# Performance work log

Measured on AMD Instinct MI355X. Metric: run time of the kernel, lower is better.

## Reference

```python
import jax, jax.numpy as jnp
import numpy as np

K = 16  # buckets per block (2**treeDepth)
DEPTH = 4

_BIT_BASE = np.array([
 [-1,-1,0,-1,0,0,0,-1,0,0,0,0,0,0,0],[-1,-1,0,-1,0,0,0,1,0,0,0,0,0,0,0],
 [-1,-1,0,1,0,0,0,0,-1,0,0,0,0,0,0],[-1,-1,0,1,0,0,0,0,1,0,0,0,0,0,0],
 [-1,1,0,0,-1,0,0,0,0,-1,0,0,0,0,0],[-1,1,0,0,-1,0,0,0,0,1,0,0,0,0,0],
 [-1,1,0,0,1,0,0,0,0,0,-1,0,0,0,0],[-1,1,0,0,1,0,0,0,0,0,1,0,0,0,0],
 [1,0,-1,0,0,-1,0,0,0,0,0,-1,0,0,0],[1,0,-1,0,0,-1,0,0,0,0,0,1,0,0,0],
 [1,0,-1,0,0,1,0,0,0,0,0,0,-1,0,0],[1,0,-1,0,0,1,0,0,0,0,0,0,1,0,0],
 [1,0,1,0,0,0,-1,0,0,0,0,0,0,-1,0],[1,0,1,0,0,0,-1,0,0,0,0,0,0,1,0],
 [1,0,1,0,0,0,1,0,0,0,0,0,0,0,-1],[1,0,1,0,0,0,1,0,0,0,0,0,0,0,1]], dtype=np.float32)

def make_tree_des_matrix(C):
    # block-diagonal, but off-blocks are ONES per the original code (init with ones)
    m = np.ones((C * K, C * (K - 1)), dtype=np.float32)
    for c in range(C):
        m[c*K:(c+1)*K, c*(K-1):(c+1)*(K-1)] = _BIT_BASE
    return jnp.asarray(m)

def make_selection_matrix(C):
    base = np.zeros((K - 1, DEPTH), dtype=np.float32)
    base[0, 0] = 1.0
    for i in range(1, K - 1):
        base[i, int(np.log2(i + 1))] = 1.0
    sel = np.zeros((C * (K - 1), C * DEPTH), dtype=np.float32)
    for c in range(C):
        sel[c*(K-1):(c+1)*(K-1), c*DEPTH:(c+1)*DEPTH] = base
    return jnp.asarray(sel)

def setup_inputs() -> dict:
    key = jax.random.key(0)
    k1, k2, k3, k4 = jax.random.split(key, 4)
    N, D, C, M = 32768, 1024, 64, 1024
    inputMatrix = jax.random.normal(k1, (N, D), dtype=jnp.float32)
    dims = jax.random.randint(k2, (C * DEPTH,), 0, D)  # gather indices into input columns
    thresholds = jax.random.normal(k3, (C * (K - 1), 1), dtype=jnp.float32)
    lut = jax.random.normal(k4, (M, C, K), dtype=jnp.float32)
    return {
        "inputMatrix": inputMatrix,
        "dims": dims,
        "thresholds": thresholds,
        "lut": lut,
        "selection_matrix": make_selection_matrix(C),
        "tree_des_mat": make_tree_des_matrix(C),
    }

def reference(inputMatrix, dims, thresholds, lut, selection_matrix, tree_des_mat):
    N = inputMatrix.shape[0]
    M, C, Kb = lut.shape
    chosen = inputMatrix[:, dims]                              # [N, C*4]
    subtracted = selection_matrix @ chosen.T - thresholds      # [C*15, N]
    tanh_h = jnp.tanh(subtracted)
    sign_ste = jnp.sign(subtracted) - jax.lax.stop_gradient(tanh_h) + tanh_h
    tree = (tree_des_mat @ sign_ste).T.reshape(N, C, Kb)       # [N, C, 16]
    soft = jax.nn.softmax(tree, axis=2)
    hard = jax.nn.one_hot(jnp.argmax(soft, axis=2), Kb, dtype=soft.dtype)
    encoded = hard - jax.lax.stop_gradient(soft) + soft        # hard-forward / soft-backward STE
    # einsum('nij,kij->nki').sum(2) == full contraction over (C, K)
    out = jnp.einsum('nck,mck->nm', encoded, lut)              # [N, M]
    return out
```

## Files before the change

kernel.cpp:

```cpp
#include <hip/hip_runtime.h>
#include <stdint.h>

#define N_ROWS 32768
#define D_DIM  1024
#define C_TREES 64
#define K_LEAF 16
#define M_OUT  1024

typedef _Float16 half8v __attribute__((ext_vector_type(8)));
typedef _Float16 half4v __attribute__((ext_vector_type(4)));

__device__ __forceinline__ void fma8(float* a, float4 v) {
    asm("v_fma_mix_f32 %0, %8, 1.0, %0 op_sel_hi:[1,0,0]\n\t"
        "v_fma_mix_f32 %1, %8, 1.0, %1 op_sel:[1,0,0] op_sel_hi:[1,0,0]\n\t"
        "v_fma_mix_f32 %2, %9, 1.0, %2 op_sel_hi:[1,0,0]\n\t"
        "v_fma_mix_f32 %3, %9, 1.0, %3 op_sel:[1,0,0] op_sel_hi:[1,0,0]\n\t"
        "v_fma_mix_f32 %4, %10, 1.0, %4 op_sel_hi:[1,0,0]\n\t"
        "v_fma_mix_f32 %5, %10, 1.0, %5 op_sel:[1,0,0] op_sel_hi:[1,0,0]\n\t"
        "v_fma_mix_f32 %6, %11, 1.0, %6 op_sel_hi:[1,0,0]\n\t"
        "v_fma_mix_f32 %7, %11, 1.0, %7 op_sel:[1,0,0] op_sel_hi:[1,0,0]"
        : "+v"(a[0]), "+v"(a[1]), "+v"(a[2]), "+v"(a[3]),
          "+v"(a[4]), "+v"(a[5]), "+v"(a[6]), "+v"(a[7])
        : "v"(v.x), "v"(v.y), "v"(v.z), "v"(v.w));
}

__global__ __launch_bounds__(256) void k_transpose(const float* __restrict__ lut,
                                                   float* __restrict__ lutT) {
    __shared__ float tile[32][33];
    int bx = blockIdx.x;
    int by = blockIdx.y;
    int tx = threadIdx.x;
    int ty = threadIdx.y;
    int src_col = bx * 32 + tx;
#pragma unroll
    for (int i = 0; i < 4; ++i) {
        int src_row = by * 32 + ty + i * 8;
        tile[ty + i * 8][tx] = lut[(size_t)src_row * 1024 + src_col];
    }
    __syncthreads();
    int dst_col = by * 32 + tx;
#pragma unroll
    for (int i = 0; i < 4; ++i) {
        int dst_row = bx * 32 + ty + i * 8;
        lutT[(size_t)dst_row * 1024 + dst_col] = tile[tx][ty + i * 8];
    }
}

__global__ __launch_bounds__(256) void k_build_ht(const float* __restrict__ lutT,
                                                  _Float16* __restrict__ Pt) {
    int j = blockIdx.x;
    int p = blockIdx.y;
    int klo = j & 15;
    int khi = j >> 4;
    int t = threadIdx.x;
    const float4* a = (const float4*)lutT + (size_t)(p * 32 + klo) * 256;
    const float4* b = (const float4*)lutT + (size_t)(p * 32 + 16 + khi) * 256;
    float4 va = a[t];
    float4 vb = b[t];
    half4v hv;
    hv.x = (_Float16)(va.x + vb.x);
    hv.y = (_Float16)(va.y + vb.y);
    hv.z = (_Float16)(va.z + vb.z);
    hv.w = (_Float16)(va.w + vb.w);
    int tile = t >> 3;
    ((half4v*)Pt)[(size_t)tile * 65536 + (size_t)(p * 256 + j) * 8 + (t & 7)] = hv;
}

__global__ __launch_bounds__(256) void k_encode2(const float* __restrict__ in,
                                                 const int* __restrict__ dims,
                                                 const float* __restrict__ th,
                                                 uint8_t* __restrict__ code) {
    __shared__ float rows[8][1028];
    __shared__ float th_s[960];
    __shared__ int   dims_s[256];
    int t = threadIdx.x;
    dims_s[t] = dims[t];
    for (int i = t; i < 960; i += 256) th_s[i] = th[i];
    int n0 = blockIdx.x * 8;
    const float4* in4 = (const float4*)(in + (size_t)n0 * 1024);
#pragma unroll
    for (int i = 0; i < 8; ++i) {
        ((float4*)&rows[i][0])[t] = in4[i * 256 + t];
    }
    __syncthreads();
    int p = t >> 3;
    int r = t & 7;
    const float* trow = &rows[r][0];
    int cA = 2 * p, cB = 2 * p + 1;

    float xA[4], xB[4];
#pragma unroll
    for (int l = 0; l < 4; ++l) {
        xA[l] = trow[dims_s[cA * 4 + l]];
        xB[l] = trow[dims_s[cB * 4 + l]];
    }
    const float* tAp = &th_s[cA * 15];
    const float* tBp = &th_s[cB * 15];
    unsigned mA = 0, mB = 0;
#pragma unroll
    for (int i = 0; i < 15; ++i) {
        const int d = (i == 0) ? 0 : (i < 3) ? 1 : (i < 7) ? 2 : 3;
        mA |= ((unsigned)(xA[d] > tAp[i])) << i;
        mB |= ((unsigned)(xB[d] > tBp[i])) << i;
    }
    int nA = 0, nB = 0;
#pragma unroll
    for (int l = 0; l < 4; ++l) {
        nA = 2 * nA + 1 + ((mA >> nA) & 1);
        nB = 2 * nB + 1 + ((mB >> nB) & 1);
    }
    code[(size_t)p * N_ROWS + n0 + r] = (uint8_t)(((nB - 15) << 4) | (nA - 15));
}

__global__ __launch_bounds__(512, 6) void k_accum6(const _Float16* __restrict__ Pt,
                                                   const uint8_t* __restrict__ code,
                                                   float* __restrict__ out) {
    __shared__ float4 sl[3][1024];

    int t  = threadIdx.x;
    int mc = t & 3;
    int ng = t >> 2;
    int tile = blockIdx.x;
    int n0 = blockIdx.y * 512;
    const float4* Pt4 = (const float4*)Pt + (size_t)tile * 32768;

    auto stage = [&](int buf, int slice) {
#pragma unroll
        for (int it = 0; it < 2; ++it) {
            int idx = t + it * 512;
            const float4* src = Pt4 + slice * 1024 + idx;
            __builtin_amdgcn_global_load_lds((const __attribute__((address_space(1))) void*)src,
                                             (__attribute__((address_space(3))) void*)(&sl[buf][idx]),
                                             16, 0, 0);
        }
    };

    float acc[4][8];
#pragma unroll
    for (int j = 0; j < 4; ++j)
#pragma unroll
        for (int q = 0; q < 8; ++q) acc[j][q] = 0.f;

    const uint8_t* cp = code + n0 + ng * 4;
    uint32_t cdE = *(const uint32_t*)cp;
    uint32_t cdO = *(const uint32_t*)(cp + N_ROWS);
    asm volatile("" ::: "memory");
    stage(0, 0);
    stage(1, 2);
    int bc = 0;

    for (int i = 0; i < 16; ++i) {
        asm volatile("s_waitcnt vmcnt(4)" ::: "memory");
        asm volatile("s_barrier" ::: "memory");

        int o = 2 * i + 1;
        float4 gv0, gv1, gv2, gv3;
        {
            int c0 = (int)(cdO & 0xff);
            int c1 = (int)((cdO >> 8) & 0xff);
            int c2 = (int)((cdO >> 16) & 0xff);
            int c3 = (int)((cdO >> 24) & 0xff);
            int ob = o << 8;
            gv0 = Pt4[(ob + c0) * 4 + mc];
            gv1 = Pt4[(ob + c1) * 4 + mc];
            gv2 = Pt4[(ob + c2) * 4 + mc];
            gv3 = Pt4[(ob + c3) * 4 + mc];
        }
        int ip = (i < 15) ? (i + 1) : 0;
        uint32_t cdE2 = *(const uint32_t*)(cp + (size_t)(2 * ip) * N_ROWS);
        uint32_t cdO2 = *(const uint32_t*)(cp + (size_t)(2 * ip + 1) * N_ROWS);
        asm volatile("" ::: "memory");
        int ns = (i < 14) ? (2 * i + 4) : 0;
        int bs = bc + 2; if (bs >= 3) bs -= 3;
        stage(bs, ns);

        const float4* s = &sl[bc][0];
#pragma unroll
        for (int j = 0; j < 4; ++j) {
            int cv = (int)((cdE >> (8 * j)) & 0xff);
            float4 v = s[cv * 4 + mc];
            fma8(acc[j], v);
        }
        fma8(acc[0], gv0);
        fma8(acc[1], gv1);
        fma8(acc[2], gv2);
        fma8(acc[3], gv3);

        cdE = cdE2; cdO = cdO2;
        bc = (bc == 2) ? 0 : bc + 1;
    }

    float4* out4 = (float4*)out;
#pragma unroll
    for (int j = 0; j < 4; ++j) {
        int n = n0 + ng * 4 + j;
        size_t base = (size_t)n * 256 + tile * 8 + mc * 2;
        out4[base]     = make_float4(acc[j][0], acc[j][1], acc[j][2], acc[j][3]);
        out4[base + 1] = make_float4(acc[j][4], acc[j][5], acc[j][6], acc[j][7]);
    }
}

__global__ __launch_bounds__(256) void k_encode(const float* __restrict__ in,
                                                const int* __restrict__ dims,
                                                const float* __restrict__ th,
                                                uint8_t* __restrict__ leaf) {
    __shared__ float rows[8][1028];
    __shared__ float th_s[960];
    __shared__ int   dims_s[256];
    int t = threadIdx.x;
    dims_s[t] = dims[t];
    for (int i = t; i < 960; i += 256) th_s[i] = th[i];
    int n0 = blockIdx.x * 8;
    const float4* in4 = (const float4*)(in + (size_t)n0 * 1024);
#pragma unroll
    for (int i = 0; i < 8; ++i) {
        ((float4*)&rows[i][0])[t] = in4[i * 256 + t];
    }
    __syncthreads();
#pragma unroll
    for (int i = 0; i < 2; ++i) {
        int id = i * 256 + t;
        int c = id >> 3;
        int r = id & 7;
        int node = 0;
        const float* trow = &rows[r][0];
#pragma unroll
        for (int lvl = 0; lvl < 4; ++lvl) {
            float x   = trow[dims_s[c * 4 + lvl]];
            float thv = th_s[c * 15 + node];
            node = 2 * node + 1 + ((x > thv) ? 1 : 0);
        }
        leaf[(size_t)c * N_ROWS + n0 + r] = (uint8_t)(node - 15);
    }
}

__global__ __launch_bounds__(512) void k_accum(const float* __restrict__ lutT,
                                               const uint8_t* __restrict__ leaf,
                                               float* __restrict__ out) {
    __shared__ float4 sl[2][16][32];
    int t     = threadIdx.x;
    int mlane = t & 31;
    int ngrp  = t >> 5;
    int wave  = t >> 6;
    int lane  = t & 63;
    int srow  = 2 * wave + (lane >> 5);
    int schunk = lane & 31;
    int m0 = blockIdx.x * 128;
    int n0 = blockIdx.y * 128;
    const float4* lutT4 = (const float4*)lutT;
    auto stage = [&](int buf, int c) {
        const float4* src = lutT4 + ((size_t)(c * 16 + srow) * 256) + (m0 >> 2) + schunk;
        __builtin_amdgcn_global_load_lds((const __attribute__((address_space(1))) void*)src,
                                         (__attribute__((address_space(3))) void*)&sl[buf][2 * wave][0],
                                         16, 0, 0);
    };
    float4 acc[8];
#pragma unroll
    for (int j = 0; j < 8; ++j) acc[j] = make_float4(0.f, 0.f, 0.f, 0.f);
    const uint8_t* lp = leaf + n0 + ngrp * 8;
    uint64_t lv = *(const uint64_t*)lp;
    stage(0, 0);
#pragma unroll 2
    for (int c = 0; c < 64; ++c) {
        __syncthreads();
        if (c < 63) stage((c + 1) & 1, c + 1);
        uint64_t lv_next = (c < 63) ? *(const uint64_t*)(lp + (size_t)(c + 1) * N_ROWS) : 0ull;
        int buf = c & 1;
#pragma unroll
        for (int j = 0; j < 8; ++j) {
            int k = (int)((lv >> (8 * j)) & 15);
            float4 v = sl[buf][k][mlane];
            acc[j].x += v.x; acc[j].y += v.y; acc[j].z += v.z; acc[j].w += v.w;
        }
        lv = lv_next;
    }
    float4* out4 = (float4*)out;
#pragma unroll
    for (int j = 0; j < 8; ++j) {
        int n = n0 + ngrp * 8 + j;
        out4[(size_t)n * 256 + (m0 >> 2) + mlane] = acc[j];
    }
}

extern "C" void kernel_launch(void* const* d_in, const int* in_sizes, int n_in,
                              void* d_out, int out_size, void* d_ws, size_t ws_size,
                              hipStream_t stream) {
    const float* inputMatrix = (const float*)d_in[0];
    const int*   dims        = (const int*)d_in[1];
    const float* thresholds  = (const float*)d_in[2];
    const float* lut         = (const float*)d_in[3];
    float* out = (float*)d_out;

    float* lutT = (float*)d_ws;

    const size_t NEED = (size_t)4 * 1024 * 1024
                      + (size_t)16 * 1024 * 1024
                      + (size_t)1 * 1024 * 1024;

    if (ws_size >= NEED) {
        _Float16* Pt   = (_Float16*)((char*)d_ws + (size_t)4 * 1024 * 1024);
        uint8_t* codep = (uint8_t*)d_ws + (size_t)20 * 1024 * 1024;

        k_transpose<<<dim3(32, 32), dim3(32, 8), 0, stream>>>(lut, lutT);
        k_build_ht<<<dim3(256, 32), 256, 0, stream>>>(lutT, Pt);
        k_encode2<<<N_ROWS / 8, 256, 0, stream>>>(inputMatrix, dims, thresholds, codep);
        k_accum6<<<dim3(M_OUT / 32, N_ROWS / 512), 512, 0, stream>>>(Pt, codep, out);
    } else {
        uint8_t* leaf = (uint8_t*)d_ws + (size_t)4 * 1024 * 1024;
        k_transpose<<<dim3(32, 32), dim3(32, 8), 0, stream>>>(lut, lutT);
        k_encode<<<N_ROWS / 8, 256, 0, stream>>>(inputMatrix, dims, thresholds, leaf);
        k_accum<<<dim3(M_OUT / 128, N_ROWS / 128), 512, 0, stream>>>(lutT, leaf, out);
    }
}
```

Before: 310.8 us.

## Pre-scale codes to 16-bit offsets and sum LDS+global pairs in fp16

The encoder now writes 16-bit codes already shifted into float4 index form, so the accumulate kernel can skip per-element shift and multiply address math and read four codes with one 64-bit load. The accumulate loop adds the LDS-staged and globally gathered half8 vectors in packed fp16 before one fused-mix FMA pass, which halves the fp32 FMA count. The wait and barrier move to the end of each iteration, with an explicit sync after the initial staging. The extra fp16 addition adds some rounding error, and the code array doubles in size.

```diff
diff --git a/kernel.cpp b/kernel.cpp
--- a/kernel.cpp
+++ b/kernel.cpp
@@ -66,10 +66,10 @@
     ((half4v*)Pt)[(size_t)tile * 65536 + (size_t)(p * 256 + j) * 8 + (t & 7)] = hv;
 }
 
-__global__ __launch_bounds__(256) void k_encode2(const float* __restrict__ in,
+__global__ __launch_bounds__(256) void k_encode3(const float* __restrict__ in,
                                                  const int* __restrict__ dims,
                                                  const float* __restrict__ th,
-                                                 uint8_t* __restrict__ code) {
+                                                 uint16_t* __restrict__ code16) {
     __shared__ float rows[8][1028];
     __shared__ float th_s[960];
     __shared__ int   dims_s[256];
@@ -109,11 +109,12 @@
         nA = 2 * nA + 1 + ((mA >> nA) & 1);
         nB = 2 * nB + 1 + ((mB >> nB) & 1);
     }
-    code[(size_t)p * N_ROWS + n0 + r] = (uint8_t)(((nB - 15) << 4) | (nA - 15));
-}
-
-__global__ __launch_bounds__(512, 6) void k_accum6(const _Float16* __restrict__ Pt,
-                                                   const uint8_t* __restrict__ code,
+    code16[(size_t)p * N_ROWS + n0 + r] =
+        (uint16_t)(((nB - 15) << 6) | ((nA - 15) << 2));
+}
+
+__global__ __launch_bounds__(512, 6) void k_accum7(const _Float16* __restrict__ Pt,
+                                                   const uint16_t* __restrict__ code16,
                                                    float* __restrict__ out) {
     __shared__ float4 sl[3][1024];
 
@@ -123,6 +124,7 @@
     int tile = blockIdx.x;
     int n0 = blockIdx.y * 512;
     const float4* Pt4 = (const float4*)Pt + (size_t)tile * 32768;
+    const float4* slf = &sl[0][0];
 
     auto stage = [&](int buf, int slice) {
 #pragma unroll
@@ -141,50 +143,50 @@
 #pragma unroll
         for (int q = 0; q < 8; ++q) acc[j][q] = 0.f;
 
-    const uint8_t* cp = code + n0 + ng * 4;
-    uint32_t cdE = *(const uint32_t*)cp;
-    uint32_t cdO = *(const uint32_t*)(cp + N_ROWS);
+    const uint16_t* cp16 = code16 + n0 + ng * 4;
+    uint64_t cdE = *(const uint64_t*)cp16;
+    uint64_t cdO = *(const uint64_t*)(cp16 + N_ROWS);
     asm volatile("" ::: "memory");
     stage(0, 0);
     stage(1, 2);
+    __syncthreads();
     int bc = 0;
 
     for (int i = 0; i < 16; ++i) {
-        asm volatile("s_waitcnt vmcnt(4)" ::: "memory");
-        asm volatile("s_barrier" ::: "memory");
-
-        int o = 2 * i + 1;
-        float4 gv0, gv1, gv2, gv3;
-        {
-            int c0 = (int)(cdO & 0xff);
-            int c1 = (int)((cdO >> 8) & 0xff);
-            int c2 = (int)((cdO >> 16) & 0xff);
-            int c3 = (int)((cdO >> 24) & 0xff);
-            int ob = o << 8;
-            gv0 = Pt4[(ob + c0) * 4 + mc];
-            gv1 = Pt4[(ob + c1) * 4 + mc];
-            gv2 = Pt4[(ob + c2) * 4 + mc];
-            gv3 = Pt4[(ob + c3) * 4 + mc];
-        }
+        const float4* Po = Pt4 + (size_t)(2 * i + 1) * 1024;
+        uint32_t oLo = (uint32_t)cdO, oHi = (uint32_t)(cdO >> 32);
+        float4 g0 = Po[(oLo & 0xffffu) | mc];
+        float4 g1 = Po[(oLo >> 16)     | mc];
+        float4 g2 = Po[(oHi & 0xffffu) | mc];
+        float4 g3 = Po[(oHi >> 16)     | mc];
+
         int ip = (i < 15) ? (i + 1) : 0;
-        uint32_t cdE2 = *(const uint32_t*)(cp + (size_t)(2 * ip) * N_ROWS);
-        uint32_t cdO2 = *(const uint32_t*)(cp + (size_t)(2 * ip + 1) * N_ROWS);
+        uint64_t cdE2 = *(const uint64_t*)(cp16 + (size_t)(2 * ip) * N_ROWS);
+        uint64_t cdO2 = *(const uint64_t*)(cp16 + (size_t)(2 * ip + 1) * N_ROWS);
         asm volatile("" ::: "memory");
+
         int ns = (i < 14) ? (2 * i + 4) : 0;
         int bs = bc + 2; if (bs >= 3) bs -= 3;
         stage(bs, ns);
 
-        const float4* s = &sl[bc][0];
-#pragma unroll
-        for (int j = 0; j < 4; ++j) {
-            int cv = (int)((cdE >> (8 * j)) & 0xff);
-            float4 v = s[cv * 4 + mc];
-            fma8(acc[j], v);
-        }
-        fma8(acc[0], gv0);
-        fma8(acc[1], gv1);
-        fma8(acc[2], gv2);
-        fma8(acc[3], gv3);
+        uint32_t eLo = (uint32_t)cdE, eHi = (uint32_t)(cdE >> 32);
+        int sbase = bc << 10;
+        float4 l0 = slf[sbase + ((eLo & 0xffffu) | mc)];
+        float4 l1 = slf[sbase + ((eLo >> 16)     | mc)];
+        float4 l2 = slf[sbase + ((eHi & 0xffffu) | mc)];
+        float4 l3 = slf[sbase + ((eHi >> 16)     | mc)];
+
+        half8v s0 = __builtin_bit_cast(half8v, l0) + __builtin_bit_cast(half8v, g0);
+        half8v s1 = __builtin_bit_cast(half8v, l1) + __builtin_bit_cast(half8v, g1);
+        half8v s2 = __builtin_bit_cast(half8v, l2) + __builtin_bit_cast(half8v, g2);
+        half8v s3 = __builtin_bit_cast(half8v, l3) + __builtin_bit_cast(half8v, g3);
+        fma8(acc[0], __builtin_bit_cast(float4, s0));
+        fma8(acc[1], __builtin_bit_cast(float4, s1));
+        fma8(acc[2], __builtin_bit_cast(float4, s2));
+        fma8(acc[3], __builtin_bit_cast(float4, s3));
+
+        asm volatile("s_waitcnt vmcnt(4)" ::: "memory");
+        asm volatile("s_barrier" ::: "memory");
 
         cdE = cdE2; cdO = cdO2;
         bc = (bc == 2) ? 0 : bc + 1;
@@ -295,16 +297,16 @@
 
     const size_t NEED = (size_t)4 * 1024 * 1024
                       + (size_t)16 * 1024 * 1024
-                      + (size_t)1 * 1024 * 1024;
+                      + (size_t)2 * 1024 * 1024;
 
     if (ws_size >= NEED) {
-        _Float16* Pt   = (_Float16*)((char*)d_ws + (size_t)4 * 1024 * 1024);
-        uint8_t* codep = (uint8_t*)d_ws + (size_t)20 * 1024 * 1024;
+        _Float16* Pt     = (_Float16*)((char*)d_ws + (size_t)4 * 1024 * 1024);
+        uint16_t* code16 = (uint16_t*)((char*)d_ws + (size_t)20 * 1024 * 1024);
 
         k_transpose<<<dim3(32, 32), dim3(32, 8), 0, stream>>>(lut, lutT);
         k_build_ht<<<dim3(256, 32), 256, 0, stream>>>(lutT, Pt);
-        k_encode2<<<N_ROWS / 8, 256, 0, stream>>>(inputMatrix, dims, thresholds, codep);
-        k_accum6<<<dim3(M_OUT / 32, N_ROWS / 512), 512, 0, stream>>>(Pt, codep, out);
+        k_encode3<<<N_ROWS / 8, 256, 0, stream>>>(inputMatrix, dims, thresholds, code16);
+        k_accum7<<<dim3(M_OUT / 32, N_ROWS / 512), 512, 0, stream>>>(Pt, code16, out);
     } else {
         uint8_t* leaf = (uint8_t*)d_ws + (size_t)4 * 1024 * 1024;
         k_transpose<<<dim3(32, 32), dim3(32, 8), 0, stream>>>(lut, lutT);
```

After: 325.9 us. 4.9% more time.
